# Kernel tuning notes

Measured on AMD Instinct MI355X. Metric: run time of the kernel, lower is better.

The kernel has to match this reference:

```python
import jax, jax.numpy as jnp
import numpy as np

B, C_IN, H, W = 4, 1536, 64, 64   # SGI input: cat of three 512-ch encoder maps at 64x64
HID, OUT = 1536, 512
N = H * W


def _grid_edge_index(h, w):
    # 4-connected bidirectional grid, matching SGI.grid_edge_index
    idx = np.arange(h * w).reshape(h, w)
    right = np.stack([idx[:, :-1].ravel(), idx[:, 1:].ravel()])
    down = np.stack([idx[:-1, :].ravel(), idx[1:, :].ravel()])
    ei = np.concatenate([right, down, right[::-1], down[::-1]], axis=1)
    return ei.astype(np.int32)


def setup_inputs() -> dict:
    key = jax.random.key(0)
    ks = jax.random.split(key, 7)
    ei = _grid_edge_index(H, W)
    s = 0.02
    return {
        "x":  jax.random.normal(ks[0], (B, C_IN, H, W), jnp.float32),
        "W1": jax.random.normal(ks[1], (C_IN, HID), jnp.float32) * s,
        "b1": jnp.zeros((HID,), jnp.float32),
        "W2": jax.random.normal(ks[2], (HID, OUT), jnp.float32) * s,
        "b2": jnp.zeros((OUT,), jnp.float32),
        "Wl": jax.random.normal(ks[3], (C_IN, OUT), jnp.float32) * s,
        "bl": jnp.zeros((OUT,), jnp.float32),
        "src": jnp.asarray(ei[0]),
        "dst": jnp.asarray(ei[1]),
    }


def _gcn(h_in, Wt, b, src, dst, inv_sqrt_deg, inv_deg):
    # PyG GCNConv: lin -> symmetric-normalized aggregation (with self loops) -> +bias
    h = h_in @ Wt                                   # [B, N, F]
    norm = inv_sqrt_deg[src] * inv_sqrt_deg[dst]    # [E]
    msgs = h[:, src, :] * norm[None, :, None]       # [B, E, F]
    # self-loop contribution has norm 1/deg_i
    agg = (h * inv_deg[None, :, None]).at[:, dst, :].add(msgs)
    return agg + b


def reference(x, W1, b1, W2, b2, Wl, bl, src, dst):
    Bb, C, Hh, Ww = x.shape
    n = Hh * Ww
    # degree including self loop (graph is symmetric)
    deg = jnp.zeros((n,), x.dtype).at[dst].add(1.0) + 1.0
    inv_sqrt_deg = jax.lax.rsqrt(deg)
    inv_deg = 1.0 / deg

    xt = x.reshape(Bb, C, n).transpose(0, 2, 1)     # [B, N, C]
    identity = xt
    origin = xt @ Wl + bl                           # [B, N, OUT]
    h = jax.nn.relu(_gcn(xt, W1, b1, src, dst, inv_sqrt_deg, inv_deg))
    h = _gcn(h + identity, W2, b2, src, dst, inv_sqrt_deg, inv_deg)
    out = h * origin                                # [B, N, OUT]
    return out.transpose(0, 2, 1).reshape(Bb, out.shape[-1], Hh, Ww)
```

## Files before the change

kernel.cpp:

```cpp
#include <hip/hip_runtime.h>
#include <hip/hip_bf16.h>
#include <stdint.h>


typedef __bf16 bf16;
typedef float f32x4 __attribute__((ext_vector_type(4)));
typedef bf16 bf16x8 __attribute__((ext_vector_type(8)));

#define NB 4
#define NN 4096
#define CIN 1536
#define HIDF 1536
#define OUTF 512

__device__ __forceinline__ float rs_of(int gx, int gy) {
  const int d = (gx > 0) + (gx < 63) + (gy > 0) + (gy < 63);
  return d == 2 ? 0.57735027f : (d == 3 ? 0.5f : 0.44721360f);
}

#define XBLK 6144
#define W1BLK 576
#define W2BLK 192

__global__ __launch_bounds__(256) void prep(
    const float* __restrict__ x, const float* __restrict__ W1,
    const float* __restrict__ W2, const float* __restrict__ Wl,
    bf16* __restrict__ xt, bf16* __restrict__ xa, bf16* __restrict__ w1t,
    bf16* __restrict__ w2t, bf16* __restrict__ wlt) {
  __shared__ float vt[64 * 64];
  __shared__ float at[64 * 64];
  const int B = blockIdx.x, t = threadIdx.x;
  const int tx = t & 15, ty = t >> 4;
  const int lane = t & 63, w = t >> 6;
  const int u = lane & 7, n3 = lane >> 3;

  if (B < XBLK) {
    const int slot = B >> 3;
    const int nt = (B & 7) * 8 + (slot & 7);
    const int ct = (slot >> 3) % 24;
    const int bb = (slot >> 3) / 24;
    const int gy = nt;
    const int n0 = nt * 64, c0 = ct * 64;
    const float* xb = x + (long)bb * CIN * NN;
    const float* rowb = xb + (long)(c0 + ty * 4) * NN + n0 + tx * 4;

    f32x4 v[4], up[4], dn[4];
#pragma unroll
    for (int cc = 0; cc < 4; cc++) v[cc] = *(const f32x4*)(rowb + (long)cc * NN);
    if (gy > 0) {
#pragma unroll
      for (int cc = 0; cc < 4; cc++)
        up[cc] = *(const f32x4*)(rowb + (long)cc * NN - 64);
    } else {
#pragma unroll
      for (int cc = 0; cc < 4; cc++) up[cc] = {0.f, 0.f, 0.f, 0.f};
    }
    if (gy < 63) {
#pragma unroll
      for (int cc = 0; cc < 4; cc++)
        dn[cc] = *(const f32x4*)(rowb + (long)cc * NN + 64);
    } else {
#pragma unroll
      for (int cc = 0; cc < 4; cc++) dn[cc] = {0.f, 0.f, 0.f, 0.f};
    }
    float lf[4], rt[4];
#pragma unroll
    for (int cc = 0; cc < 4; cc++) {
      lf[cc] = __shfl_up(v[cc][3], 1);
      rt[cc] = __shfl_down(v[cc][0], 1);
    }

#pragma unroll
    for (int cc = 0; cc < 4; cc++) {
      const int cl = ty * 4 + cc;
      const int nb = tx * 4;
      f32x4 a;
#pragma unroll
      for (int i = 0; i < 4; i++) {
        const int gx = nb + i;
        const float rs_s = rs_of(gx, gy);
        const float lv = (i == 0) ? lf[cc] : v[cc][i - 1];
        const float rv = (i == 3) ? rt[cc] : v[cc][i + 1];
        float sum = v[cc][i] * rs_s;
        if (gx > 0) sum += lv * rs_of(gx - 1, gy);
        if (gx < 63) sum += rv * rs_of(gx + 1, gy);
        if (gy > 0) sum += up[cc][i] * rs_of(gx, gy - 1);
        if (gy < 63) sum += dn[cc][i] * rs_of(gx, gy + 1);
        a[i] = rs_s * sum;
      }
      const int chunk = tx ^ (2 * ((cl >> 3) & 7));
      *(f32x4*)&vt[cl * 64 + chunk * 4] = v[cc];
      *(f32x4*)&at[cl * 64 + chunk * 4] = a;
    }
    __syncthreads();
    bf16* xtb = xt + (long)bb * NN * CIN;
    bf16* xab = xa + (long)bb * NN * CIN;
#pragma unroll
    for (int q = 0; q < 4; q++) {
      const int j = q * 4 + w;
      const int arr = j & 1, r = j >> 1;
      const int nl = n3 + 8 * r;
      const float* s = arr ? at : vt;
      bf16x8 o;
#pragma unroll
      for (int jj = 0; jj < 8; jj++) {
        const int cl = u * 8 + jj;
        const int col = nl ^ (8 * ((cl >> 3) & 7));
        o[jj] = (bf16)s[cl * 64 + col];
      }
      bf16* outp = arr ? xab : xtb;
      *(bf16x8*)&outp[(long)(n0 + nl) * CIN + c0 + u * 8] = o;
    }
  } else {
    int B2 = B - XBLK;
    const float* srcp;
    bf16* dstp;
    int Fdim, Kd, nt, ct;
    if (B2 < W1BLK) {
      nt = B2 / 24; ct = B2 % 24; srcp = W1; dstp = w1t; Fdim = HIDF; Kd = CIN;
    } else if (B2 < W1BLK + W2BLK) {
      const int l = B2 - W1BLK;
      nt = l / 24; ct = l % 24; srcp = W2; dstp = w2t; Fdim = OUTF; Kd = HIDF;
    } else {
      const int l = B2 - W1BLK - W2BLK;
      nt = l / 24; ct = l % 24; srcp = Wl; dstp = wlt; Fdim = OUTF; Kd = CIN;
    }
    const int n0 = nt * 64, c0 = ct * 64;
#pragma unroll
    for (int cc = 0; cc < 4; cc++) {
      const int cl = ty * 4 + cc;
      const float* row = srcp + (long)(c0 + cl) * Fdim + n0;
      f32x4 v = *(const f32x4*)(row + tx * 4);
      const int chunk = tx ^ (2 * ((cl >> 3) & 7));
      *(f32x4*)&vt[cl * 64 + chunk * 4] = v;
    }
    __syncthreads();
#pragma unroll
    for (int q = 0; q < 2; q++) {
      const int r = q * 4 + w;
      const int nl = n3 + 8 * r;
      bf16x8 o;
#pragma unroll
      for (int jj = 0; jj < 8; jj++) {
        const int cl = u * 8 + jj;
        const int col = nl ^ (8 * ((cl >> 3) & 7));
        o[jj] = (bf16)vt[cl * 64 + col];
      }
      *(bf16x8*)&dstp[(long)(n0 + nl) * Kd + c0 + u * 8] = o;
    }
  }
}

__device__ __forceinline__ void async_copy16(const void* g, void* l) {
  __builtin_amdgcn_global_load_lds(
      (const __attribute__((address_space(1))) void*)g,
      (__attribute__((address_space(3))) void*)l, 16, 0, 0);
}

struct GemmCtx {
  f32x4 acc[4][4];
  int wave, lane, wm, wn, quad, l15;
};

__device__ __forceinline__ void gemm_init(GemmCtx& cx, int t) {
  cx.wave = t >> 6;
  cx.lane = t & 63;
  cx.wm = (cx.wave & 1) * 64;
  cx.wn = (cx.wave >> 1) * 64;
  cx.quad = cx.lane >> 4;
  cx.l15 = cx.lane & 15;
#pragma unroll
  for (int i = 0; i < 4; i++)
#pragma unroll
    for (int j = 0; j < 4; j++) cx.acc[i][j] = {0.f, 0.f, 0.f, 0.f};
}

template <int K>
__device__ __forceinline__ void gemm_kloop(GemmCtx& cx, const bf16* Ab,
                                           const bf16* Bb, bf16* As,
                                           bf16* Bs) {
  const int r = cx.lane >> 3, c8 = cx.lane & 7;
  const int fchunk = c8 ^ r;
  constexpr int NT = K / 64;
#pragma unroll
  for (int i = 0; i < 4; i++) {
    const int row = i * 32 + cx.wave * 8;
    async_copy16(Ab + (long)(row + r) * K + fchunk * 8, &As[row * 64]);
    async_copy16(Bb + (long)(row + r) * K + fchunk * 8, &Bs[row * 64]);
  }
  __syncthreads();
#pragma unroll 2
  for (int t = 0; t < NT; ++t) {
    const int cur = (t & 1) * (128 * 64);
    const int nxt = cur ^ (128 * 64);
    const int ktn = ((t + 1 < NT) ? t + 1 : t) * 64;
#pragma unroll
    for (int i = 0; i < 4; i++) {
      const int row = i * 32 + cx.wave * 8;
      async_copy16(Ab + (long)(row + r) * K + ktn + fchunk * 8,
                   &As[nxt + row * 64]);
      async_copy16(Bb + (long)(row + r) * K + ktn + fchunk * 8,
                   &Bs[nxt + row * 64]);
    }
#pragma unroll
    for (int kk = 0; kk < 2; kk++) {
      const int q = kk * 4 + cx.quad;
      bf16x8 af[4], bfv[4];
#pragma unroll
      for (int mr = 0; mr < 4; mr++) {
        const int m = cx.wm + mr * 16 + cx.l15;
        af[mr] = *(const bf16x8*)&As[cur + m * 64 + (q ^ (m & 7)) * 8];
      }
#pragma unroll
      for (int nc = 0; nc < 4; nc++) {
        const int n = cx.wn + nc * 16 + cx.l15;
        bfv[nc] = *(const bf16x8*)&Bs[cur + n * 64 + (q ^ (n & 7)) * 8];
      }
#pragma unroll
      for (int mr = 0; mr < 4; mr++)
#pragma unroll
        for (int nc = 0; nc < 4; nc++)
          cx.acc[mr][nc] = __builtin_amdgcn_mfma_f32_16x16x32_bf16(
              af[mr], bfv[nc], cx.acc[mr][nc], 0, 0, 0);
    }
    __syncthreads();
  }
}

__global__ __launch_bounds__(256) void gemm_h(
    const bf16* __restrict__ xa, const bf16* __restrict__ w1t,
    const bf16* __restrict__ xt, bf16* __restrict__ h,
    const float* __restrict__ b1, int nbase) {
  __shared__ bf16 As[2 * 128 * 64];
  __shared__ bf16 Bs[2 * 128 * 64];
  GemmCtx cx;
  gemm_init(cx, threadIdx.x);
  const int m0 = blockIdx.x * 128, n0 = nbase + blockIdx.y * 128;
  const int z = blockIdx.z;
  gemm_kloop<CIN>(cx, xa + (long)z * NN * CIN + (long)m0 * CIN,
                  w1t + (long)n0 * CIN, As, Bs);
  const bf16* Xb = xt + (long)z * NN * HIDF;
  bf16* Cb = h + (long)z * NN * HIDF;
#pragma unroll
  for (int mr = 0; mr < 4; mr++)
#pragma unroll
    for (int nc = 0; nc < 4; nc++) {
      const int gn = n0 + cx.wn + nc * 16 + cx.l15;
      const float bv = b1[gn];
#pragma unroll
      for (int j = 0; j < 4; j++) {
        const int gm = m0 + cx.wm + mr * 16 + cx.quad * 4 + j;
        float v = cx.acc[mr][nc][j] + bv;
        v = v > 0.f ? v : 0.f;
        Cb[(long)gm * HIDF + gn] = (bf16)(v + (float)Xb[(long)gm * HIDF + gn]);
      }
    }
}

template <bool ADD_BIAS>
__global__ __launch_bounds__(256) void gemm_f32(
    const bf16* __restrict__ A, const bf16* __restrict__ Bw,
    float* __restrict__ C, const float* __restrict__ bias) {
  __shared__ bf16 As[2 * 128 * 64];
  __shared__ bf16 Bs[2 * 128 * 64];
  GemmCtx cx;
  gemm_init(cx, threadIdx.x);
  const int m0 = blockIdx.x * 128, n0 = blockIdx.y * 128, z = blockIdx.z;
  gemm_kloop<CIN>(cx, A + (long)z * NN * CIN + (long)m0 * CIN,
                  Bw + (long)n0 * CIN, As, Bs);
  float* Cb = C + (long)z * NN * OUTF;
#pragma unroll
  for (int mr = 0; mr < 4; mr++)
#pragma unroll
    for (int nc = 0; nc < 4; nc++) {
      const int gn = n0 + cx.wn + nc * 16 + cx.l15;
      float bv = 0.f;
      if (ADD_BIAS) bv = bias[gn];
#pragma unroll
      for (int j = 0; j < 4; j++) {
        const int gm = m0 + cx.wm + mr * 16 + cx.quad * 4 + j;
        Cb[(long)gm * OUTF + gn] = cx.acc[mr][nc][j] + bv;
      }
    }
}

__global__ __launch_bounds__(256) void stencil2(
    const float* __restrict__ G2, const float* __restrict__ Orig,
    const float* __restrict__ b2, float* __restrict__ out) {
  __shared__ float tile[16][516];
  const int blk = blockIdx.x;
  const int s = ((blk & 7) << 5) + (blk >> 3);
  const int n0 = s * 16, b = blockIdx.y;
  const int t = threadIdx.x;
  const int fq = t & 127, nl = t >> 7;
  const int f = fq * 4;
  const f32x4 bv = *(const f32x4*)(b2 + f);
#pragma unroll
  for (int p = 0; p < 8; p++) {
    const int nLoc = p * 2 + nl;
    const int n = n0 + nLoc;
    const int gx = n & 63, gy = n >> 6;
    const float rs_n = rs_of(gx, gy);
    const long rb = ((long)b * NN + n) * (long)OUTF + f;
    f32x4 g = *(const f32x4*)(G2 + rb);
    f32x4 a;
#pragma unroll
    for (int i = 0; i < 4; i++) a[i] = g[i] * rs_n;
    if (gx > 0) {
      const float w = rs_of(gx - 1, gy);
      f32x4 u = *(const f32x4*)(G2 + rb - OUTF);
#pragma unroll
      for (int i = 0; i < 4; i++) a[i] += u[i] * w;
    }
    if (gx < 63) {
      const float w = rs_of(gx + 1, gy);
      f32x4 u = *(const f32x4*)(G2 + rb + OUTF);
#pragma unroll
      for (int i = 0; i < 4; i++) a[i] += u[i] * w;
    }
    if (gy > 0) {
      const float w = rs_of(gx, gy - 1);
      f32x4 u = *(const f32x4*)(G2 + rb - 64L * OUTF);
#pragma unroll
      for (int i = 0; i < 4; i++) a[i] += u[i] * w;
    }
    if (gy < 63) {
      const float w = rs_of(gx, gy + 1);
      f32x4 u = *(const f32x4*)(G2 + rb + 64L * OUTF);
#pragma unroll
      for (int i = 0; i < 4; i++) a[i] += u[i] * w;
    }
    f32x4 og = *(const f32x4*)(Orig + rb);
    f32x4 res;
#pragma unroll
    for (int i = 0; i < 4; i++) res[i] = (a[i] * rs_n + bv[i]) * og[i];
    *(f32x4*)&tile[nLoc][f] = res;
  }
  __syncthreads();
  const int j = t & 3, fr = t >> 2;
#pragma unroll
  for (int q = 0; q < 8; q++) {
    const int ff = q * 64 + fr;
    f32x4 v;
#pragma unroll
    for (int k = 0; k < 4; k++) v[k] = tile[j * 4 + k][ff];
    *(f32x4*)&out[((long)b * OUTF + ff) * (long)NN + n0 + j * 4] = v;
  }
}

extern "C" void kernel_launch(void* const* d_in, const int* in_sizes, int n_in,
                              void* d_out, int out_size, void* d_ws,
                              size_t ws_size, hipStream_t stream) {
  const float* x = (const float*)d_in[0];
  const float* W1 = (const float*)d_in[1];
  const float* b1 = (const float*)d_in[2];
  const float* W2 = (const float*)d_in[3];
  const float* b2 = (const float*)d_in[4];
  const float* Wl = (const float*)d_in[5];
  const float* bl = (const float*)d_in[6];
  float* out = (float*)d_out;

  uint8_t* ws = (uint8_t*)d_ws;
  size_t off = 0;
  auto alloc = [&](size_t bytes) -> void* {
    void* p = ws + off;
    off += (bytes + 255) & ~(size_t)255;
    return p;
  };
  bf16* xt = (bf16*)alloc((size_t)NB * NN * CIN * 2);
  bf16* xa = (bf16*)alloc((size_t)NB * NN * CIN * 2);
  bf16* hb = (bf16*)alloc((size_t)NB * NN * HIDF * 2);
  bf16* w1t = (bf16*)alloc((size_t)HIDF * CIN * 2);
  bf16* w2t = (bf16*)alloc((size_t)OUTF * HIDF * 2);
  bf16* wlt = (bf16*)alloc((size_t)OUTF * CIN * 2);
  float* origin = (float*)xa;
  float* g2 = (float*)xt;

  prep<<<XBLK + W1BLK + 2 * W2BLK, 256, 0, stream>>>(x, W1, W2, Wl, xt, xa,
                                                     w1t, w2t, wlt);
  gemm_h<<<dim3(NN / 128, 4, NB), 256, 0, stream>>>(xa, w1t, xt, hb, b1, 0);
  gemm_h<<<dim3(NN / 128, 4, NB), 256, 0, stream>>>(xa, w1t, xt, hb, b1, 512);
  gemm_h<<<dim3(NN / 128, 4, NB), 256, 0, stream>>>(xa, w1t, xt, hb, b1, 1024);
  gemm_f32<true><<<dim3(NN / 128, OUTF / 128, NB), 256, 0, stream>>>(
      xt, wlt, origin, bl);
  gemm_f32<false><<<dim3(NN / 128, OUTF / 128, NB), 256, 0, stream>>>(
      hb, w2t, g2, nullptr);
  stencil2<<<dim3(256, NB), 256, 0, stream>>>(g2, origin, b2, out);
}
```

Before: 367.0 us.

## Reuse halo rows across four grid rows in prep and merge gemm_h launches

Each prep block for x now walks four consecutive grid rows and keeps rolling up/current/down register buffers, so every row of x is loaded about once instead of three times for the vertical stencil. The next row is prefetched while the current row is written out through shared memory. The three gemm_h launches over column slices are merged into one launch covering all of HIDF. The price is fewer, longer prep blocks with two barriers per row, and a single larger gemm grid.

```diff
diff --git a/kernel.cpp b/kernel.cpp
--- a/kernel.cpp
+++ b/kernel.cpp
@@ -18,7 +18,7 @@
   return d == 2 ? 0.57735027f : (d == 3 ? 0.5f : 0.44721360f);
 }
 
-#define XBLK 6144
+#define XBLK 1536
 #define W1BLK 576
 #define W2BLK 192
 
@@ -35,81 +35,103 @@
   const int u = lane & 7, n3 = lane >> 3;
 
   if (B < XBLK) {
-    const int slot = B >> 3;
-    const int nt = (B & 7) * 8 + (slot & 7);
-    const int ct = (slot >> 3) % 24;
-    const int bb = (slot >> 3) / 24;
-    const int gy = nt;
-    const int n0 = nt * 64, c0 = ct * 64;
+    const int yb = (B & 7) * 2 + ((B >> 3) & 1);
+    const int rest = B >> 4;
+    const int ct = rest % 24, bb = rest / 24;
+    const int c0 = ct * 64;
     const float* xb = x + (long)bb * CIN * NN;
-    const float* rowb = xb + (long)(c0 + ty * 4) * NN + n0 + tx * 4;
-
-    f32x4 v[4], up[4], dn[4];
-#pragma unroll
-    for (int cc = 0; cc < 4; cc++) v[cc] = *(const f32x4*)(rowb + (long)cc * NN);
-    if (gy > 0) {
-#pragma unroll
-      for (int cc = 0; cc < 4; cc++)
-        up[cc] = *(const f32x4*)(rowb + (long)cc * NN - 64);
-    } else {
-#pragma unroll
-      for (int cc = 0; cc < 4; cc++) up[cc] = {0.f, 0.f, 0.f, 0.f};
-    }
-    if (gy < 63) {
-#pragma unroll
-      for (int cc = 0; cc < 4; cc++)
-        dn[cc] = *(const f32x4*)(rowb + (long)cc * NN + 64);
-    } else {
-#pragma unroll
-      for (int cc = 0; cc < 4; cc++) dn[cc] = {0.f, 0.f, 0.f, 0.f};
-    }
-    float lf[4], rt[4];
-#pragma unroll
-    for (int cc = 0; cc < 4; cc++) {
-      lf[cc] = __shfl_up(v[cc][3], 1);
-      rt[cc] = __shfl_down(v[cc][0], 1);
-    }
-
-#pragma unroll
-    for (int cc = 0; cc < 4; cc++) {
-      const int cl = ty * 4 + cc;
-      const int nb = tx * 4;
-      f32x4 a;
-#pragma unroll
-      for (int i = 0; i < 4; i++) {
-        const int gx = nb + i;
-        const float rs_s = rs_of(gx, gy);
-        const float lv = (i == 0) ? lf[cc] : v[cc][i - 1];
-        const float rv = (i == 3) ? rt[cc] : v[cc][i + 1];
-        float sum = v[cc][i] * rs_s;
-        if (gx > 0) sum += lv * rs_of(gx - 1, gy);
-        if (gx < 63) sum += rv * rs_of(gx + 1, gy);
-        if (gy > 0) sum += up[cc][i] * rs_of(gx, gy - 1);
-        if (gy < 63) sum += dn[cc][i] * rs_of(gx, gy + 1);
-        a[i] = rs_s * sum;
-      }
-      const int chunk = tx ^ (2 * ((cl >> 3) & 7));
-      *(f32x4*)&vt[cl * 64 + chunk * 4] = v[cc];
-      *(f32x4*)&at[cl * 64 + chunk * 4] = a;
-    }
-    __syncthreads();
+    const float* rowb = xb + (long)(c0 + ty * 4) * NN + tx * 4;
     bf16* xtb = xt + (long)bb * NN * CIN;
     bf16* xab = xa + (long)bb * NN * CIN;
-#pragma unroll
-    for (int q = 0; q < 4; q++) {
-      const int j = q * 4 + w;
-      const int arr = j & 1, r = j >> 1;
-      const int nl = n3 + 8 * r;
-      const float* s = arr ? at : vt;
-      bf16x8 o;
-#pragma unroll
-      for (int jj = 0; jj < 8; jj++) {
-        const int cl = u * 8 + jj;
-        const int col = nl ^ (8 * ((cl >> 3) & 7));
-        o[jj] = (bf16)s[cl * 64 + col];
-      }
-      bf16* outp = arr ? xab : xtb;
-      *(bf16x8*)&outp[(long)(n0 + nl) * CIN + c0 + u * 8] = o;
+
+    f32x4 vup[4], vcur[4], vdn[4];
+    const int gy0 = yb * 4;
+    if (gy0 > 0) {
+#pragma unroll
+      for (int cc = 0; cc < 4; cc++)
+        vup[cc] = *(const f32x4*)(rowb + (long)cc * NN + (long)(gy0 - 1) * 64);
+    } else {
+#pragma unroll
+      for (int cc = 0; cc < 4; cc++) vup[cc] = {0.f, 0.f, 0.f, 0.f};
+    }
+#pragma unroll
+    for (int cc = 0; cc < 4; cc++)
+      vcur[cc] = *(const f32x4*)(rowb + (long)cc * NN + (long)gy0 * 64);
+#pragma unroll
+    for (int cc = 0; cc < 4; cc++)
+      vdn[cc] = *(const f32x4*)(rowb + (long)cc * NN + (long)(gy0 + 1) * 64);
+
+#pragma unroll
+    for (int s = 0; s < 4; s++) {
+      const int gy = yb * 4 + s;
+      const int n0 = gy * 64;
+      float lf[4], rt[4];
+#pragma unroll
+      for (int cc = 0; cc < 4; cc++) {
+        lf[cc] = __shfl_up(vcur[cc][3], 1);
+        rt[cc] = __shfl_down(vcur[cc][0], 1);
+      }
+#pragma unroll
+      for (int cc = 0; cc < 4; cc++) {
+        const int cl = ty * 4 + cc;
+        const int nb = tx * 4;
+        f32x4 a;
+#pragma unroll
+        for (int i = 0; i < 4; i++) {
+          const int gx = nb + i;
+          const float rs_s = rs_of(gx, gy);
+          const float lv = (i == 0) ? lf[cc] : vcur[cc][i - 1];
+          const float rv = (i == 3) ? rt[cc] : vcur[cc][i + 1];
+          float sum = vcur[cc][i] * rs_s;
+          if (gx > 0) sum += lv * rs_of(gx - 1, gy);
+          if (gx < 63) sum += rv * rs_of(gx + 1, gy);
+          if (gy > 0) sum += vup[cc][i] * rs_of(gx, gy - 1);
+          if (gy < 63) sum += vdn[cc][i] * rs_of(gx, gy + 1);
+          a[i] = rs_s * sum;
+        }
+        const int chunk = tx ^ (2 * ((cl >> 3) & 7));
+        *(f32x4*)&vt[cl * 64 + chunk * 4] = vcur[cc];
+        *(f32x4*)&at[cl * 64 + chunk * 4] = a;
+      }
+      f32x4 vnext[4];
+      if (s < 3) {
+        const int gn = gy + 2;
+        if (gn <= 63) {
+#pragma unroll
+          for (int cc = 0; cc < 4; cc++)
+            vnext[cc] =
+                *(const f32x4*)(rowb + (long)cc * NN + (long)gn * 64);
+        } else {
+#pragma unroll
+          for (int cc = 0; cc < 4; cc++) vnext[cc] = {0.f, 0.f, 0.f, 0.f};
+        }
+      }
+      __syncthreads();
+#pragma unroll
+      for (int q = 0; q < 4; q++) {
+        const int j = q * 4 + w;
+        const int arr = j & 1, r2 = j >> 1;
+        const int nl = n3 + 8 * r2;
+        const float* sp = arr ? at : vt;
+        bf16x8 o;
+#pragma unroll
+        for (int jj = 0; jj < 8; jj++) {
+          const int cl = u * 8 + jj;
+          const int col = nl ^ (8 * ((cl >> 3) & 7));
+          o[jj] = (bf16)sp[cl * 64 + col];
+        }
+        bf16* outp = arr ? xab : xtb;
+        *(bf16x8*)&outp[(long)(n0 + nl) * CIN + c0 + u * 8] = o;
+      }
+      if (s < 3) {
+        __syncthreads();
+#pragma unroll
+        for (int cc = 0; cc < 4; cc++) {
+          vup[cc] = vcur[cc];
+          vcur[cc] = vdn[cc];
+          vdn[cc] = vnext[cc];
+        }
+      }
     }
   } else {
     int B2 = B - XBLK;
@@ -230,13 +252,12 @@
 __global__ __launch_bounds__(256) void gemm_h(
     const bf16* __restrict__ xa, const bf16* __restrict__ w1t,
     const bf16* __restrict__ xt, bf16* __restrict__ h,
-    const float* __restrict__ b1, int nbase) {
+    const float* __restrict__ b1) {
   __shared__ bf16 As[2 * 128 * 64];
   __shared__ bf16 Bs[2 * 128 * 64];
   GemmCtx cx;
   gemm_init(cx, threadIdx.x);
-  const int m0 = blockIdx.x * 128, n0 = nbase + blockIdx.y * 128;
-  const int z = blockIdx.z;
+  const int m0 = blockIdx.x * 128, n0 = blockIdx.y * 128, z = blockIdx.z;
   gemm_kloop<CIN>(cx, xa + (long)z * NN * CIN + (long)m0 * CIN,
                   w1t + (long)n0 * CIN, As, Bs);
   const bf16* Xb = xt + (long)z * NN * HIDF;
@@ -378,9 +399,8 @@
 
   prep<<<XBLK + W1BLK + 2 * W2BLK, 256, 0, stream>>>(x, W1, W2, Wl, xt, xa,
                                                      w1t, w2t, wlt);
-  gemm_h<<<dim3(NN / 128, 4, NB), 256, 0, stream>>>(xa, w1t, xt, hb, b1, 0);
-  gemm_h<<<dim3(NN / 128, 4, NB), 256, 0, stream>>>(xa, w1t, xt, hb, b1, 512);
-  gemm_h<<<dim3(NN / 128, 4, NB), 256, 0, stream>>>(xa, w1t, xt, hb, b1, 1024);
+  gemm_h<<<dim3(NN / 128, HIDF / 128, NB), 256, 0, stream>>>(xa, w1t, xt, hb,
+                                                             b1);
   gemm_f32<true><<<dim3(NN / 128, OUTF / 128, NB), 256, 0, stream>>>(
       xt, wlt, origin, bl);
   gemm_f32<false><<<dim3(NN / 128, OUTF / 128, NB), 256, 0, stream>>>(
```

Result: no change. 370.2 us (+0.9%).
